# Optimization experiments

Measured on AMD Instinct MI355X. Metric: run time of the kernel, lower is better.

## Reference

```python
import jax, jax.numpy as jnp
import numpy as np

MODEL_DIM = 2048
NUM_HEADS = 32
HEAD_DIM = 64
NUM_KV_HEADS = 8
ROPE_BASE = 10000.0
BATCH = 2
SEQ = 2048


def setup_inputs() -> dict:
    key = jax.random.key(0)
    ks = jax.random.split(key, 5)
    sd = 1.0 / np.sqrt(MODEL_DIM)
    x = jax.random.normal(ks[0], (BATCH, SEQ, MODEL_DIM), dtype=jnp.float32)
    Wq = jax.random.normal(ks[1], (MODEL_DIM, NUM_HEADS * HEAD_DIM), dtype=jnp.float32) * sd
    Wk = jax.random.normal(ks[2], (MODEL_DIM, NUM_KV_HEADS * HEAD_DIM), dtype=jnp.float32) * sd
    Wv = jax.random.normal(ks[3], (MODEL_DIM, NUM_KV_HEADS * HEAD_DIM), dtype=jnp.float32) * sd
    Wo = jax.random.normal(ks[4], (NUM_HEADS * HEAD_DIM, MODEL_DIM), dtype=jnp.float32) * sd
    return {"x": x, "Wq": Wq, "Wk": Wk, "Wv": Wv, "Wo": Wo}


def _rope_cache(seq_len, head_dim, base, dtype):
    # inv_freq over even dims, standard rotate-half (Llama-style) RoPE cache
    inv_freq = 1.0 / (base ** (jnp.arange(0, head_dim, 2, dtype=jnp.float32) / head_dim))
    t = jnp.arange(seq_len, dtype=jnp.float32)
    freqs = jnp.outer(t, inv_freq)               # [S, hd/2]
    emb = jnp.concatenate([freqs, freqs], axis=-1)  # [S, hd]
    return jnp.cos(emb).astype(dtype), jnp.sin(emb).astype(dtype)


def _rotate_half(x):
    h = x.shape[-1] // 2
    return jnp.concatenate([-x[..., h:], x[..., :h]], axis=-1)


def _apply_rope(q, k, cos, sin):
    # q,k: [B, H, S, hd]; cos,sin: [S, hd] -> broadcast over batch/heads
    cos = cos[None, None, :, :]
    sin = sin[None, None, :, :]
    q = q * cos + _rotate_half(q) * sin
    k = k * cos + _rotate_half(k) * sin
    return q, k


def reference(x, Wq, Wk, Wv, Wo):
    bsz, seq_len, _ = x.shape
    q_per_kv = NUM_HEADS // NUM_KV_HEADS

    # projections -> [B, H, S, hd]
    q = (x @ Wq).reshape(bsz, seq_len, NUM_HEADS, HEAD_DIM).transpose(0, 2, 1, 3)
    k = (x @ Wk).reshape(bsz, seq_len, NUM_KV_HEADS, HEAD_DIM).transpose(0, 2, 1, 3)
    v = (x @ Wv).reshape(bsz, seq_len, NUM_KV_HEADS, HEAD_DIM).transpose(0, 2, 1, 3)

    # GQA: repeat_interleave KV heads to match Q heads
    k = jnp.repeat(k, q_per_kv, axis=1)
    v = jnp.repeat(v, q_per_kv, axis=1)

    cos, sin = _rope_cache(seq_len, HEAD_DIM, ROPE_BASE, x.dtype)
    q, k = _apply_rope(q, k, cos, sin)

    scale = 1.0 / np.sqrt(HEAD_DIM)
    scores = jnp.einsum('bhqd,bhkd->bhqk', q, k) * scale  # [B,H,S,S]
    causal = jnp.tril(jnp.ones((seq_len, seq_len), dtype=bool))
    scores = jnp.where(causal[None, None], scores, jnp.finfo(scores.dtype).min)
    attn = jax.nn.softmax(scores, axis=-1)
    y = jnp.einsum('bhqk,bhkd->bhqd', attn, v)  # [B,H,S,hd]

    y = y.transpose(0, 2, 1, 3).reshape(bsz, seq_len, NUM_HEADS * HEAD_DIM)
    return y @ Wo
```

## Files before the change

kernel.cpp:

```cpp
#include <hip/hip_runtime.h>
#include <cstdint>

typedef unsigned short u16;
typedef __attribute__((ext_vector_type(8))) short short8;
typedef __attribute__((ext_vector_type(4))) short short4v;
typedef __attribute__((ext_vector_type(4))) float f32x4;

#define SEQ     2048
#define NHEADS  32
#define NKV     8
#define HD      64
#define DM      2048
#define MROWS   4096
#define KVSTR   1024
#define PSTR    88

__device__ __forceinline__ float b2f(unsigned int u) {
    return __builtin_bit_cast(float, u << 16);
}
__device__ __forceinline__ u16 f2b(float f) {
    unsigned int u = __builtin_bit_cast(unsigned int, f);
    return (u16)((u + 0x7fffu + ((u >> 16) & 1u)) >> 16);
}

#define GLOAD_LDS16(g, l)                                              \
    __builtin_amdgcn_global_load_lds(                                  \
        (const __attribute__((address_space(1))) void*)(g),            \
        (__attribute__((address_space(3))) void*)(l), 16, 0, 0)

__global__ __launch_bounds__(256) void cvt_f32_bf16(
    const float* __restrict__ in, u16* __restrict__ out, int n4) {
    int i = blockIdx.x * 256 + threadIdx.x;
    if (i < n4) {
        float4 v = ((const float4*)in)[i];
        ushort4 o;
        o.x = f2b(v.x); o.y = f2b(v.y); o.z = f2b(v.z); o.w = f2b(v.w);
        ((ushort4*)out)[i] = o;
    }
}

__global__ __launch_bounds__(256) void rope_table_kernel(
    float* __restrict__ cosT, float* __restrict__ sinT) {
    int idx = blockIdx.x * 256 + threadIdx.x;
    int s  = idx >> 5;
    int dl = idx & 31;
    float inv_freq = exp2f((float)dl * -0.41524101186092025f);
    float ang = (float)s * inv_freq;
    float sn, cs;
    sincosf(ang, &sn, &cs);
    cosT[idx] = cs;
    sinT[idx] = sn;
}

__global__ __launch_bounds__(256) void transpose_f32_bf16(
    const float* __restrict__ in, u16* __restrict__ out, int K, int N) {
    __shared__ float tile[32][33];
    int n0 = blockIdx.x * 32, k0 = blockIdx.y * 32;
    int tx = threadIdx.x, ty = threadIdx.y;
    for (int r = ty; r < 32; r += 8)
        tile[r][tx] = in[(size_t)(k0 + r) * N + n0 + tx];
    __syncthreads();
    for (int r = ty; r < 32; r += 8)
        out[(size_t)(n0 + r) * K + k0 + tx] = f2b(tile[tx][r]);
}

#define GEMM_BODY(A, BT, Kdim)                                             \
    constexpr int BK = 32;                                                 \
    __shared__ __align__(16) u16 As[128 * BK];                             \
    __shared__ __align__(16) u16 Bs[128 * BK];                             \
    const int tid  = threadIdx.x;                                          \
    const int wid  = tid >> 6;                                             \
    const int lane = tid & 63;                                             \
    const int quad = lane >> 4;                                            \
    const int l16  = lane & 15;                                            \
    const int rowBase = blockIdx.y * 128;                                  \
    const int colBase = blockIdx.x * 128;                                  \
    const int wr = (wid >> 1) * 64;                                        \
    const int wc = (wid & 1) * 64;                                         \
    const int srow = wid * 32 + (lane >> 2);                               \
    const int scol = (lane & 3) * 8;                                       \
    const u16* gA = (A)  + (size_t)(rowBase + srow) * (Kdim) + scol;       \
    const u16* gB = (BT) + (size_t)(colBase + srow) * (Kdim) + scol;       \
    u16* lA0 = &As[(wid * 32) * BK];                                       \
    u16* lA1 = &As[(wid * 32 + 16) * BK];                                  \
    u16* lB0 = &Bs[(wid * 32) * BK];                                       \
    u16* lB1 = &Bs[(wid * 32 + 16) * BK];                                  \
    const size_t row16 = (size_t)16 * (Kdim);                              \
    f32x4 acc[4][4] = {};                                                  \
    for (int k0 = 0; k0 < (Kdim); k0 += BK) {                              \
        GLOAD_LDS16(gA + k0,         lA0);                                 \
        GLOAD_LDS16(gA + k0 + row16, lA1);                                 \
        GLOAD_LDS16(gB + k0,         lB0);                                 \
        GLOAD_LDS16(gB + k0 + row16, lB1);                                 \
        __syncthreads();                                                   \
        short8 a[4], b[4];                                                 \
        _Pragma("unroll")                                                  \
        for (int mi = 0; mi < 4; ++mi)                                     \
            a[mi] = *(const short8*)&As[(wr + mi * 16 + l16) * BK + quad * 8]; \
        _Pragma("unroll")                                                  \
        for (int ni = 0; ni < 4; ++ni)                                     \
            b[ni] = *(const short8*)&Bs[(wc + ni * 16 + l16) * BK + quad * 8]; \
        _Pragma("unroll")                                                  \
        for (int mi = 0; mi < 4; ++mi)                                     \
            _Pragma("unroll")                                              \
            for (int ni = 0; ni < 4; ++ni)                                 \
                acc[mi][ni] = __builtin_amdgcn_mfma_f32_16x16x32_bf16(     \
                    a[mi], b[ni], acc[mi][ni], 0, 0, 0);                   \
        __syncthreads();                                                   \
    }                                                                      \
    const int wRow = rowBase + wr;                                         \
    const int wCol = colBase + wc;

__global__ __launch_bounds__(256) void gemm_qkv(
    const u16* __restrict__ A, const u16* __restrict__ BT,
    u16* __restrict__ Qb, u16* __restrict__ KVb,
    const float* __restrict__ cosT, const float* __restrict__ sinT) {
    GEMM_BODY(A, BT, DM)

    u16* dst;
    int dstride, dcol;
    float scale;
    bool doRope;
    if (wCol < 2048)      { dst = Qb;  dstride = 2048; dcol = wCol;        scale = 0.125f; doRope = true;  }
    else if (wCol < 2560) { dst = KVb; dstride = 1024; dcol = wCol - 2048; scale = 1.0f;   doRope = true;  }
    else                  { dst = KVb; dstride = 1024; dcol = wCol - 2048; scale = 1.0f;   doRope = false; }

#pragma unroll
    for (int mi = 0; mi < 4; ++mi) {
#pragma unroll
        for (int r = 0; r < 4; ++r) {
            const int R = wRow + mi * 16 + quad * 4 + r;
            u16* crow = dst + (size_t)R * dstride + dcol;
            if (doRope) {
                const int s = R & (SEQ - 1);
#pragma unroll
                for (int ni = 0; ni < 2; ++ni) {
                    const int dl = ni * 16 + l16;
                    float lo = acc[mi][ni][r];
                    float hi = acc[mi][ni + 2][r];
                    float cs = cosT[s * 32 + dl];
                    float sn = sinT[s * 32 + dl];
                    crow[dl]      = f2b((lo * cs - hi * sn) * scale);
                    crow[dl + 32] = f2b((hi * cs + lo * sn) * scale);
                }
            } else {
#pragma unroll
                for (int ni = 0; ni < 4; ++ni)
                    crow[ni * 16 + l16] = f2b(acc[mi][ni][r]);
            }
        }
    }
}

__global__ __launch_bounds__(256) void gemm_out(
    const u16* __restrict__ A, const u16* __restrict__ BT,
    float* __restrict__ C32) {
    GEMM_BODY(A, BT, DM)
#pragma unroll
    for (int mi = 0; mi < 4; ++mi) {
#pragma unroll
        for (int r = 0; r < 4; ++r) {
            const int R = wRow + mi * 16 + quad * 4 + r;
            float* crow = C32 + (size_t)R * DM + wCol;
#pragma unroll
            for (int ni = 0; ni < 4; ++ni)
                crow[ni * 16 + l16] = acc[mi][ni][r];
        }
    }
}

__global__ __launch_bounds__(512, 4) void flash_attn(
    const u16* __restrict__ Q, const u16* __restrict__ KV,
    u16* __restrict__ Y) {
    __shared__ __align__(16) u16 Ks[64 * 64];
    __shared__ __align__(16) u16 Vt[64 * 72];
    __shared__ __align__(16) u16 Ps[8 * 16 * PSTR];

    const int h   = blockIdx.y;
    const int b   = blockIdx.z;
    const int kvh = h >> 2;
    const int tid  = threadIdx.x;
    const int wid  = tid >> 6;
    const int lane = tid & 63;
    const int quad = lane >> 4;
    const int l16  = lane & 15;

    const u16* Kg = KV + (size_t)b * SEQ * KVSTR + kvh * HD;
    const u16* Vg = Kg + 512;
    u16* Psw = Ps + wid * 16 * PSTR;

    const int kKey = tid >> 3, kCc = tid & 7;
    const int vkp  = tid & 31;
    const int vd0  = (tid >> 5) * 4;

    for (int half = 0; half < 2; ++half) {
        const int qt = half ? (15 - blockIdx.x) : blockIdx.x;
        const int rowBaseW = qt * 128 + wid * 16;

        short8 qf[2];
#pragma unroll
        for (int ks = 0; ks < 2; ++ks)
            qf[ks] = *(const short8*)&Q[
                (size_t)(b * SEQ + rowBaseW + l16) * (NHEADS * HD)
                + h * HD + ks * 32 + quad * 8];

        f32x4 o[4] = {};
        float mi[4], li[4];
#pragma unroll
        for (int r = 0; r < 4; ++r) { mi[r] = -3e38f; li[r] = 0.f; }

        const int nTiles = 2 * qt + 2;

        short8  kreg = *(const short8*)&Kg[(size_t)kKey * KVSTR + kCc * 8];
        short4v vrA  = *(const short4v*)&Vg[(size_t)(2 * vkp)     * KVSTR + vd0];
        short4v vrB  = *(const short4v*)&Vg[(size_t)(2 * vkp + 1) * KVSTR + vd0];

        for (int t = 0; t < nTiles; ++t) {
            const int j0 = t * 64;
            __syncthreads();

            *(short8*)&Ks[kKey * 64 + ((kCc ^ (kKey & 7)) * 8)] = kreg;
#pragma unroll
            for (int i = 0; i < 4; ++i) {
                unsigned int w = (unsigned int)(u16)vrA[i]
                               | ((unsigned int)(u16)vrB[i] << 16);
                ((unsigned int*)Vt)[(vd0 + i) * 36 + vkp] = w;
            }
            __syncthreads();

            if (t + 1 < nTiles) {
                const size_t jn = (size_t)(j0 + 64);
                kreg = *(const short8*)&Kg[(jn + kKey) * KVSTR + kCc * 8];
                vrA  = *(const short4v*)&Vg[(jn + 2 * vkp)     * KVSTR + vd0];
                vrB  = *(const short4v*)&Vg[(jn + 2 * vkp + 1) * KVSTR + vd0];
            }

            f32x4 s[4] = {};
#pragma unroll
            for (int ks = 0; ks < 2; ++ks)
#pragma unroll
                for (int ct = 0; ct < 4; ++ct) {
                    int key = ct * 16 + l16;
                    int cc  = (ks * 4 + quad) ^ (key & 7);
                    short8 bk = *(const short8*)&Ks[key * 64 + cc * 8];
                    s[ct] = __builtin_amdgcn_mfma_f32_16x16x32_bf16(
                        qf[ks], bk, s[ct], 0, 0, 0);
                }

            if (j0 + 63 > rowBaseW) {
#pragma unroll
                for (int ct = 0; ct < 4; ++ct)
#pragma unroll
                    for (int r = 0; r < 4; ++r) {
                        int R = rowBaseW + quad * 4 + r;
                        int J = j0 + ct * 16 + l16;
                        if (J > R) s[ct][r] = -3e38f;
                    }
            }

#pragma unroll
            for (int r = 0; r < 4; ++r) {
                float rmax = fmaxf(fmaxf(s[0][r], s[1][r]),
                                   fmaxf(s[2][r], s[3][r]));
                rmax = fmaxf(rmax, __shfl_xor(rmax, 1, 64));
                rmax = fmaxf(rmax, __shfl_xor(rmax, 2, 64));
                rmax = fmaxf(rmax, __shfl_xor(rmax, 4, 64));
                rmax = fmaxf(rmax, __shfl_xor(rmax, 8, 64));
                float mnew  = fmaxf(mi[r], rmax);
                float alpha = __expf(mi[r] - mnew);
                mi[r] = mnew;
                float rs = 0.f;
#pragma unroll
                for (int ct = 0; ct < 4; ++ct) {
                    float p = __expf(s[ct][r] - mnew);
                    s[ct][r] = p;
                    rs += p;
                    o[ct][r] *= alpha;
                }
                rs += __shfl_xor(rs, 1, 64);
                rs += __shfl_xor(rs, 2, 64);
                rs += __shfl_xor(rs, 4, 64);
                rs += __shfl_xor(rs, 8, 64);
                li[r] = li[r] * alpha + rs;
            }

#pragma unroll
            for (int ct = 0; ct < 4; ++ct)
#pragma unroll
                for (int r = 0; r < 4; ++r)
                    Psw[(quad * 4 + r) * PSTR + ct * 16 + l16] = f2b(s[ct][r]);

            short8 pa[2];
#pragma unroll
            for (int ks = 0; ks < 2; ++ks)
                pa[ks] = *(const short8*)&Psw[l16 * PSTR + ks * 32 + quad * 8];
#pragma unroll
            for (int ks = 0; ks < 2; ++ks)
#pragma unroll
                for (int ct = 0; ct < 4; ++ct) {
                    short8 vbf = *(const short8*)&Vt[(ct * 16 + l16) * 72 + ks * 32 + quad * 8];
                    o[ct] = __builtin_amdgcn_mfma_f32_16x16x32_bf16(
                        pa[ks], vbf, o[ct], 0, 0, 0);
                }
        }

        float rli[4];
#pragma unroll
        for (int r = 0; r < 4; ++r) rli[r] = 1.0f / li[r];
#pragma unroll
        for (int r = 0; r < 4; ++r) {
            int R = rowBaseW + quad * 4 + r;
            u16* yrow = Y + (size_t)(b * SEQ + R) * (NHEADS * HD) + h * HD;
#pragma unroll
            for (int ct = 0; ct < 4; ++ct)
                yrow[ct * 16 + l16] = f2b(o[ct][r] * rli[r]);
        }
    }
}

extern "C" void kernel_launch(void* const* d_in, const int* in_sizes, int n_in,
                              void* d_out, int out_size, void* d_ws, size_t ws_size,
                              hipStream_t stream) {
    const float* x  = (const float*)d_in[0];
    const float* Wq = (const float*)d_in[1];
    const float* Wk = (const float*)d_in[2];
    const float* Wv = (const float*)d_in[3];
    const float* Wo = (const float*)d_in[4];
    float* out = (float*)d_out;

    char* ws = (char*)d_ws;
    u16*  xb    = (u16*)(ws);
    u16*  WqkvT = (u16*)(ws + 16777216);
    u16*  WoT   = (u16*)(ws + 29360128);
    u16*  Qb    = (u16*)(ws + 37748736);
    u16*  KVb   = (u16*)(ws + 54525952);
    u16*  Yb    = (u16*)(ws + 62914560);
    float* cosT = (float*)(ws + 79691776);
    float* sinT = (float*)(ws + 79953920);

    rope_table_kernel<<<dim3(65536 / 256), 256, 0, stream>>>(cosT, sinT);

    cvt_f32_bf16<<<dim3(MROWS * DM / 4 / 256), 256, 0, stream>>>(x, xb, MROWS * DM / 4);

    dim3 tb(32, 8);
    transpose_f32_bf16<<<dim3(2048/32, 2048/32), tb, 0, stream>>>(Wq, WqkvT, 2048, 2048);
    transpose_f32_bf16<<<dim3( 512/32, 2048/32), tb, 0, stream>>>(Wk, WqkvT + 2048 * 2048, 2048, 512);
    transpose_f32_bf16<<<dim3( 512/32, 2048/32), tb, 0, stream>>>(Wv, WqkvT + 2560 * 2048, 2048, 512);
    transpose_f32_bf16<<<dim3(2048/32, 2048/32), tb, 0, stream>>>(Wo, WoT, 2048, 2048);

    gemm_qkv<<<dim3(24, 32), 256, 0, stream>>>(xb, WqkvT, Qb, KVb, cosT, sinT);

    flash_attn<<<dim3(8, NHEADS, 2), 512, 0, stream>>>(Qb, KVb, Yb);

    gemm_out<<<dim3(16, 32), 256, 0, stream>>>(Yb, WoT, out);
}
```

Baseline: 389.8 us.

## Split attention KV range across two blocks and merge with combine kernel

Each flash-attention block pair now splits the key range of its query tiles into two halves, doubling the grid to 1024 blocks. One half writes fp32 partial outputs and the other writes bf16 partials, and each records per-row max and sum. A new combine kernel merges the two halves with softmax rescaling. The aim is more parallelism and occupancy on the attention stage, paid for by an extra kernel launch, additional global traffic for the partials, and a bf16 rounding of one partial before combining. The Wo transpose is moved after attention so the workspace it overwrites (reused for the partials) is free.

```diff
diff --git a/kernel.cpp b/kernel.cpp
--- a/kernel.cpp
+++ b/kernel.cpp
@@ -171,11 +171,14 @@
 
 __global__ __launch_bounds__(512, 4) void flash_attn(
     const u16* __restrict__ Q, const u16* __restrict__ KV,
-    u16* __restrict__ Y) {
+    u16* __restrict__ Yb, float* __restrict__ PoA,
+    float* __restrict__ Ml) {
     __shared__ __align__(16) u16 Ks[64 * 64];
     __shared__ __align__(16) u16 Vt[64 * 72];
     __shared__ __align__(16) u16 Ps[8 * 16 * PSTR];
 
+    const int p   = blockIdx.x >> 1;
+    const int sh  = blockIdx.x & 1;
     const int h   = blockIdx.y;
     const int b   = blockIdx.z;
     const int kvh = h >> 2;
@@ -193,8 +196,10 @@
     const int vkp  = tid & 31;
     const int vd0  = (tid >> 5) * 4;
 
-    for (int half = 0; half < 2; ++half) {
-        const int qt = half ? (15 - blockIdx.x) : blockIdx.x;
+    for (int ph = 0; ph < 2; ++ph) {
+        const int qt = ph ? (15 - p) : p;
+        const int hc = ph ? (16 - p) : (p + 1);
+        const int tS = sh * hc;
         const int rowBaseW = qt * 128 + wid * 16;
 
         short8 qf[2];
@@ -209,14 +214,13 @@
 #pragma unroll
         for (int r = 0; r < 4; ++r) { mi[r] = -3e38f; li[r] = 0.f; }
 
-        const int nTiles = 2 * qt + 2;
-
-        short8  kreg = *(const short8*)&Kg[(size_t)kKey * KVSTR + kCc * 8];
-        short4v vrA  = *(const short4v*)&Vg[(size_t)(2 * vkp)     * KVSTR + vd0];
-        short4v vrB  = *(const short4v*)&Vg[(size_t)(2 * vkp + 1) * KVSTR + vd0];
-
-        for (int t = 0; t < nTiles; ++t) {
-            const int j0 = t * 64;
+        const size_t jF = (size_t)tS * 64;
+        short8  kreg = *(const short8*)&Kg[(jF + kKey) * KVSTR + kCc * 8];
+        short4v vrA  = *(const short4v*)&Vg[(jF + 2 * vkp)     * KVSTR + vd0];
+        short4v vrB  = *(const short4v*)&Vg[(jF + 2 * vkp + 1) * KVSTR + vd0];
+
+        for (int tt = 0; tt < hc; ++tt) {
+            const int j0 = (tS + tt) * 64;
             __syncthreads();
 
             *(short8*)&Ks[kKey * 64 + ((kCc ^ (kKey & 7)) * 8)] = kreg;
@@ -228,7 +232,7 @@
             }
             __syncthreads();
 
-            if (t + 1 < nTiles) {
+            if (tt + 1 < hc) {
                 const size_t jn = (size_t)(j0 + 64);
                 kreg = *(const short8*)&Kg[(jn + kKey) * KVSTR + kCc * 8];
                 vrA  = *(const short4v*)&Vg[(jn + 2 * vkp)     * KVSTR + vd0];
@@ -272,9 +276,9 @@
                 float rs = 0.f;
 #pragma unroll
                 for (int ct = 0; ct < 4; ++ct) {
-                    float p = __expf(s[ct][r] - mnew);
-                    s[ct][r] = p;
-                    rs += p;
+                    float pv = __expf(s[ct][r] - mnew);
+                    s[ct][r] = pv;
+                    rs += pv;
                     o[ct][r] *= alpha;
                 }
                 rs += __shfl_xor(rs, 1, 64);
@@ -306,16 +310,63 @@
 
         float rli[4];
 #pragma unroll
-        for (int r = 0; r < 4; ++r) rli[r] = 1.0f / li[r];
-#pragma unroll
-        for (int r = 0; r < 4; ++r) {
-            int R = rowBaseW + quad * 4 + r;
-            u16* yrow = Y + (size_t)(b * SEQ + R) * (NHEADS * HD) + h * HD;
-#pragma unroll
-            for (int ct = 0; ct < 4; ++ct)
-                yrow[ct * 16 + l16] = f2b(o[ct][r] * rli[r]);
+        for (int r = 0; r < 4; ++r)
+            rli[r] = li[r] > 0.f ? 1.0f / li[r] : 0.f;
+        if (sh == 0) {
+#pragma unroll
+            for (int r = 0; r < 4; ++r) {
+                int R = rowBaseW + quad * 4 + r;
+                float* arow = PoA + (size_t)(b * SEQ + R) * (NHEADS * HD) + h * HD;
+#pragma unroll
+                for (int ct = 0; ct < 4; ++ct)
+                    arow[ct * 16 + l16] = o[ct][r] * rli[r];
+            }
+        } else {
+#pragma unroll
+            for (int r = 0; r < 4; ++r) {
+                int R = rowBaseW + quad * 4 + r;
+                u16* yrow = Yb + (size_t)(b * SEQ + R) * (NHEADS * HD) + h * HD;
+#pragma unroll
+                for (int ct = 0; ct < 4; ++ct)
+                    yrow[ct * 16 + l16] = f2b(o[ct][r] * rli[r]);
+            }
+        }
+        if (l16 == 0) {
+            float2* MlX = (float2*)Ml + (size_t)sh * 131072
+                        + ((b * 32 + h) * 2048 + rowBaseW + quad * 4);
+#pragma unroll
+            for (int r = 0; r < 4; ++r)
+                MlX[r] = make_float2(mi[r], li[r]);
         }
     }
+}
+
+__global__ __launch_bounds__(256) void combine_kernel(
+    const float* __restrict__ PoA, const float* __restrict__ Ml,
+    u16* __restrict__ Yb) {
+    const size_t e = ((size_t)blockIdx.x * 256 + threadIdx.x) * 8;
+    const int rowg = (int)(e >> 11);
+    const int c    = (int)(e & 2047);
+    const int h    = c >> 6;
+    const int bz   = rowg >> 11;
+    const int row  = rowg & 2047;
+    const int slot = ((bz * 32 + h) * 2048 + row) * 2;
+    const float mA = Ml[slot],          lA = Ml[slot + 1];
+    const float mB = Ml[262144 + slot], lB = Ml[262144 + slot + 1];
+    const float m  = fmaxf(mA, mB);
+    const float wA = lA * __expf(mA - m);
+    const float wB = lB * __expf(mB - m);
+    const float inv = 1.0f / (wA + wB);
+    const float a = wA * inv, bw = wB * inv;
+    float4 A0 = *(const float4*)(PoA + e);
+    float4 A1 = *(const float4*)(PoA + e + 4);
+    short8 Bv = *(const short8*)(Yb + e);
+    float av[8] = {A0.x, A0.y, A0.z, A0.w, A1.x, A1.y, A1.z, A1.w};
+    u16 yo[8];
+#pragma unroll
+    for (int j = 0; j < 8; ++j)
+        yo[j] = f2b(a * av[j] + bw * b2f((unsigned int)(u16)Bv[j]));
+    *(short8*)(Yb + e) = *(short8*)yo;
 }
 
 extern "C" void kernel_launch(void* const* d_in, const int* in_sizes, int n_in,
@@ -337,6 +388,8 @@
     u16*  Yb    = (u16*)(ws + 62914560);
     float* cosT = (float*)(ws + 79691776);
     float* sinT = (float*)(ws + 79953920);
+    float* PoA  = (float*)(ws);
+    float* Ml   = (float*)(ws + 33554432);
 
     rope_table_kernel<<<dim3(65536 / 256), 256, 0, stream>>>(cosT, sinT);
 
@@ -346,11 +399,14 @@
     transpose_f32_bf16<<<dim3(2048/32, 2048/32), tb, 0, stream>>>(Wq, WqkvT, 2048, 2048);
     transpose_f32_bf16<<<dim3( 512/32, 2048/32), tb, 0, stream>>>(Wk, WqkvT + 2048 * 2048, 2048, 512);
     transpose_f32_bf16<<<dim3( 512/32, 2048/32), tb, 0, stream>>>(Wv, WqkvT + 2560 * 2048, 2048, 512);
+
+    gemm_qkv<<<dim3(24, 32), 256, 0, stream>>>(xb, WqkvT, Qb, KVb, cosT, sinT);
+
+    flash_attn<<<dim3(16, NHEADS, 2), 512, 0, stream>>>(Qb, KVb, Yb, PoA, Ml);
+
+    combine_kernel<<<dim3(4096), 256, 0, stream>>>(PoA, Ml, Yb);
+
     transpose_f32_bf16<<<dim3(2048/32, 2048/32), tb, 0, stream>>>(Wo, WoT, 2048, 2048);
 
-    gemm_qkv<<<dim3(24, 32), 256, 0, stream>>>(xb, WqkvT, Qb, KVb, cosT, sinT);
-
-    flash_attn<<<dim3(8, NHEADS, 2), 512, 0, stream>>>(Qb, KVb, Yb);
-
     gemm_out<<<dim3(16, 32), 256, 0, stream>>>(Yb, WoT, out);
 }
```

Result: slower. 403.1 us (+3.4%).
